# Kernel optimization log

Measured on AMD Instinct MI355X. Metric: run time of the kernel, lower is better.

The kernel has to match this reference:

```python
import jax, jax.numpy as jnp
import numpy as np

NUM_HEADS = 8
EPS = 1e-8

def setup_inputs() -> dict:
    key = jax.random.key(0)
    k1, k2, k3 = jax.random.split(key, 3)
    batch, L, dim = 2, 2048, 512
    B = jax.random.normal(k1, (batch, L, dim), dtype=jnp.float32)
    C = jax.random.normal(k2, (batch, L, dim), dtype=jnp.float32)
    S = jax.random.uniform(k3, (batch, L, dim), dtype=jnp.float32)
    return {"B": B, "C": C, "S": S}

def reference(B, C, S):
    batch, L, dim = B.shape
    H = NUM_HEADS
    d = dim // H
    # [b, H, L, d]
    Bh = B.reshape(batch, L, H, d).transpose(0, 2, 1, 3)
    Ch = C.reshape(batch, L, H, d).transpose(0, 2, 1, 3)
    Ah = S.reshape(batch, L, H, d).transpose(0, 2, 1, 3)
    # cum_A[0] = 1, cum_A[i] = prod_{k=1..i} A_k  (matches torch loop)
    cum_A = jnp.cumprod(Ah.at[:, :, 0, :].set(1.0), axis=2)
    ones = jnp.ones_like(cum_A[:, :, :1])
    # P[i] = cum_A[i-1] (P[0]=1): numerator of the product between j and i
    P = jnp.concatenate([ones, cum_A[:, :, :-1]], axis=2)
    # D[j] = cum_A[j-1] + eps for j>=1, D[0]=1 (j==0 branch has no eps)
    D = jnp.concatenate([ones, cum_A[:, :, :-1] + EPS], axis=2)
    # T_ij = sum_d C_i P_i B_j / D_j   for j < i
    T = jnp.einsum('bhid,bhjd->bhij', Ch * P, Bh / D)
    diag_vals = jnp.sum(Ch * Bh, axis=-1)  # T_ii = C_i . B_i
    idx = jnp.arange(L)
    strict_lower = idx[:, None] > idx[None, :]
    T = jnp.where(strict_lower, T, 0.0)
    T = T + diag_vals[:, :, :, None] * jnp.eye(L, dtype=T.dtype)
    # causal masking of strict upper triangle is already zero; use_softmax=False
    return T
```

## Files before the change

### kernel.cpp

```cpp
#include <hip/hip_runtime.h>
#include <hip/hip_bf16.h>

#define LL   2048
#define DIM  512
#define HD   64
#define BHN  16
#define NC   64
#define CH   32
#define EPSF 1e-8f

typedef __attribute__((ext_vector_type(8))) short bf16x8;
typedef __attribute__((ext_vector_type(4))) float f32x4;

__global__ __launch_bounds__(64) void chunkprod_kernel(const float* __restrict__ S,
                                                       float* __restrict__ U) {
    int c = blockIdx.x, bh = blockIdx.y;
    int b = bh >> 3, h = bh & 7;
    int d = threadIdx.x;
    int l0 = c * CH;
    size_t base = ((size_t)b * LL + l0) * DIM + h * HD + d;
    float p = 1.0f;
    for (int l = 0; l < CH; ++l) {
        float a = S[base + (size_t)l * DIM];
        if (l0 + l >= 1) p *= a;
    }
    U[((size_t)bh * NC + c) * HD + d] = p;
}

__global__ __launch_bounds__(64) void chunkscan_kernel(const float* __restrict__ U,
                                                       float* __restrict__ St) {
    int bh = blockIdx.x;
    int d = threadIdx.x;
    float p = 1.0f;
    for (int c = 0; c < NC; ++c) {
        size_t o = ((size_t)bh * NC + c) * HD + d;
        St[o] = p;
        p *= U[o];
    }
}

__global__ __launch_bounds__(64) void apply_kernel(const float* __restrict__ Bg,
                                                   const float* __restrict__ Cg,
                                                   const float* __restrict__ S,
                                                   const float* __restrict__ St,
                                                   __hip_bfloat16* __restrict__ X,
                                                   __hip_bfloat16* __restrict__ Y,
                                                   float* __restrict__ diag) {
    int c = blockIdx.x, bh = blockIdx.y;
    int b = bh >> 3, h = bh & 7;
    int d = threadIdx.x;
    int l0 = c * CH;
    size_t gbase = ((size_t)b * LL + l0) * DIM + h * HD + d;
    float p = St[((size_t)bh * NC + c) * HD + d];
    for (int l = 0; l < CH; ++l) {
        int gl = l0 + l;
        size_t gi = gbase + (size_t)l * DIM;
        float a = S[gi], bv = Bg[gi], cv = Cg[gi];
        float Dv = (gl == 0) ? 1.0f : (p + EPSF);
        size_t o = ((size_t)bh * LL + gl) * HD + d;
        X[o] = __float2bfloat16(cv * p);
        Y[o] = __float2bfloat16(bv / Dv);
        float tsum = cv * bv;
        #pragma unroll
        for (int off = 1; off < 64; off <<= 1) tsum += __shfl_xor(tsum, off);
        if (d == 0) diag[(size_t)bh * LL + gl] = tsum;
        if (gl >= 1) p *= a;
    }
}

__global__ __launch_bounds__(256) void gemm_kernel(const __hip_bfloat16* __restrict__ X,
                                                   const __hip_bfloat16* __restrict__ Y,
                                                   const float* __restrict__ diag,
                                                   float* __restrict__ out) {
    int tj = blockIdx.x, ti = blockIdx.y, bh = blockIdx.z;
    size_t obase = (size_t)bh * LL * LL;
    int i0 = ti * 128, j0 = tj * 128;
    int t = threadIdx.x;

    if (tj > ti) {
        float4 z = make_float4(0.f, 0.f, 0.f, 0.f);
        int col4 = t & 31, row0 = t >> 5;
        float* ob = out + obase + (size_t)i0 * LL + j0;
        #pragma unroll
        for (int r = 0; r < 16; ++r)
            *((float4*)(ob + (size_t)(row0 + 8 * r) * LL) + col4) = z;
        return;
    }

    __shared__ short Xs[128 * 64];
    __shared__ short Ys[128 * 64];

    {
        const float4* Xg4 = (const float4*)(X + ((size_t)bh * LL + i0) * HD);
        const float4* Yg4 = (const float4*)(Y + ((size_t)bh * LL + j0) * HD);
        int chunk = t & 7, r0 = t >> 3;
        int sc = (chunk ^ (r0 & 7)) * 8;
        #pragma unroll
        for (int p = 0; p < 4; ++p) {
            int row = r0 + 32 * p;
            float4 vx = Xg4[row * 8 + chunk];
            float4 vy = Yg4[row * 8 + chunk];
            *(float4*)&Xs[row * 64 + sc] = vx;
            *(float4*)&Ys[row * 64 + sc] = vy;
        }
    }
    __syncthreads();

    int lane = t & 63, wv = t >> 6;
    int wi = wv >> 1, wj = wv & 1;
    int l15 = lane & 15, q = lane >> 4;

    f32x4 acc[4][4] = {};
    #pragma unroll
    for (int kc = 0; kc < 2; ++kc) {
        bf16x8 af[4], bf[4];
        #pragma unroll
        for (int mt = 0; mt < 4; ++mt) {
            int row = 64 * wi + 16 * mt + l15;
            int sc = ((4 * kc + q) ^ (row & 7)) * 8;
            af[mt] = *(const bf16x8*)&Xs[row * 64 + sc];
        }
        #pragma unroll
        for (int nt = 0; nt < 4; ++nt) {
            int row = 64 * wj + 16 * nt + l15;
            int sc = ((4 * kc + q) ^ (row & 7)) * 8;
            bf[nt] = *(const bf16x8*)&Ys[row * 64 + sc];
        }
        #pragma unroll
        for (int mt = 0; mt < 4; ++mt)
            #pragma unroll
            for (int nt = 0; nt < 4; ++nt)
                acc[mt][nt] = __builtin_amdgcn_mfma_f32_16x16x32_bf16(
                    af[mt], bf[nt], acc[mt][nt], 0, 0, 0);
    }

    int i_base = i0 + 64 * wi, j_base = j0 + 64 * wj;
    if (tj < ti) {
        #pragma unroll
        for (int mt = 0; mt < 4; ++mt)
            #pragma unroll
            for (int reg = 0; reg < 4; ++reg) {
                int gi = i_base + 16 * mt + 4 * q + reg;
                float* ob = out + obase + (size_t)gi * LL + j_base;
                #pragma unroll
                for (int nt = 0; nt < 4; ++nt)
                    ob[16 * nt + l15] = acc[mt][nt][reg];
            }
    } else {
        #pragma unroll
        for (int mt = 0; mt < 4; ++mt)
            #pragma unroll
            for (int reg = 0; reg < 4; ++reg) {
                int gi = i_base + 16 * mt + 4 * q + reg;
                float dv = diag[(size_t)bh * LL + gi];
                float* ob = out + obase + (size_t)gi * LL + j_base;
                #pragma unroll
                for (int nt = 0; nt < 4; ++nt) {
                    int gj = j_base + 16 * nt + l15;
                    float v = acc[mt][nt][reg];
                    ob[16 * nt + l15] = (gj < gi) ? v : ((gj == gi) ? dv : 0.f);
                }
            }
    }
}

extern "C" void kernel_launch(void* const* d_in, const int* in_sizes, int n_in,
                              void* d_out, int out_size, void* d_ws, size_t ws_size,
                              hipStream_t stream) {
    const float* Bg = (const float*)d_in[0];
    const float* Cg = (const float*)d_in[1];
    const float* S  = (const float*)d_in[2];
    float* out = (float*)d_out;

    char* ws = (char*)d_ws;
    size_t xy_bytes = (size_t)BHN * LL * HD * sizeof(__hip_bfloat16);
    __hip_bfloat16* X = (__hip_bfloat16*)(ws);
    __hip_bfloat16* Y = (__hip_bfloat16*)(ws + xy_bytes);
    float* diag = (float*)(ws + 2 * xy_bytes);
    float* U    = (float*)(ws + 2 * xy_bytes + (size_t)BHN * LL * sizeof(float));
    float* St   = (float*)(ws + 2 * xy_bytes + (size_t)BHN * LL * sizeof(float)
                              + (size_t)BHN * NC * HD * sizeof(float));

    chunkprod_kernel<<<dim3(NC, BHN), 64, 0, stream>>>(S, U);
    chunkscan_kernel<<<BHN, 64, 0, stream>>>(U, St);
    apply_kernel<<<dim3(NC, BHN), 64, 0, stream>>>(Bg, Cg, S, St, X, Y, diag);
    gemm_kernel<<<dim3(16, 16, BHN), 256, 0, stream>>>(X, Y, diag, out);
}
```

Before: 329.1 us.

## Halve scan chunk size, parallelize chunk scan, split diag kernel, use nontemporal stores

Halves the chunk length and doubles the chunk count so the prefix and apply passes expose more blocks. The serial chunk scan becomes a two-level scan over 1024 threads using shared memory. The diagonal dot product moves out of apply_kernel into its own kernel, which adds a launch and a second read of B and C. Output stores in the GEMM, including the zero tiles, become nontemporal so the 256MB output write-out does not pollute the cache.

```diff
diff --git a/kernel.cpp b/kernel.cpp
--- a/kernel.cpp
+++ b/kernel.cpp
@@ -5,12 +5,20 @@
 #define DIM  512
 #define HD   64
 #define BHN  16
-#define NC   64
-#define CH   32
+#define NC   128
+#define CH   16
+#define GC   8
 #define EPSF 1e-8f
 
 typedef __attribute__((ext_vector_type(8))) short bf16x8;
 typedef __attribute__((ext_vector_type(4))) float f32x4;
+
+__device__ __forceinline__ void nt_store(float* p, float v) {
+    __builtin_nontemporal_store(v, p);
+}
+__device__ __forceinline__ void nt_store4(f32x4* p, f32x4 v) {
+    __builtin_nontemporal_store(v, p);
+}
 
 __global__ __launch_bounds__(64) void chunkprod_kernel(const float* __restrict__ S,
                                                        float* __restrict__ U) {
@@ -20,6 +28,7 @@
     int l0 = c * CH;
     size_t base = ((size_t)b * LL + l0) * DIM + h * HD + d;
     float p = 1.0f;
+    #pragma unroll
     for (int l = 0; l < CH; ++l) {
         float a = S[base + (size_t)l * DIM];
         if (l0 + l >= 1) p *= a;
@@ -27,16 +36,43 @@
     U[((size_t)bh * NC + c) * HD + d] = p;
 }
 
-__global__ __launch_bounds__(64) void chunkscan_kernel(const float* __restrict__ U,
-                                                       float* __restrict__ St) {
+__global__ __launch_bounds__(1024) void chunkscan_kernel(const float* __restrict__ U,
+                                                         float* __restrict__ St) {
     int bh = blockIdx.x;
-    int d = threadIdx.x;
-    float p = 1.0f;
-    for (int c = 0; c < NC; ++c) {
-        size_t o = ((size_t)bh * NC + c) * HD + d;
-        St[o] = p;
-        p *= U[o];
-    }
+    int t = threadIdx.x;
+    int g = t >> 6, d = t & 63;
+    int c0 = g * GC;
+    float u[GC];
+    float prod = 1.0f;
+    #pragma unroll
+    for (int k = 0; k < GC; ++k) {
+        u[k] = U[((size_t)bh * NC + c0 + k) * HD + d];
+        prod *= u[k];
+    }
+    __shared__ float Ls[16][64];
+    Ls[g][d] = prod;
+    __syncthreads();
+    float run = 1.0f;
+    for (int gg = 0; gg < g; ++gg) run *= Ls[gg][d];
+    #pragma unroll
+    for (int k = 0; k < GC; ++k) {
+        St[((size_t)bh * NC + c0 + k) * HD + d] = run;
+        run *= u[k];
+    }
+}
+
+__global__ __launch_bounds__(256) void diag_kernel(const float* __restrict__ Bg,
+                                                   const float* __restrict__ Cg,
+                                                   float* __restrict__ diag) {
+    int w = threadIdx.x >> 6, lane = threadIdx.x & 63;
+    int flat = blockIdx.x * 4 + w;
+    int bh = flat >> 11, l = flat & (LL - 1);
+    int b = bh >> 3, h = bh & 7;
+    size_t gi = ((size_t)b * LL + l) * DIM + h * HD + lane;
+    float tsum = Cg[gi] * Bg[gi];
+    #pragma unroll
+    for (int off = 1; off < 64; off <<= 1) tsum += __shfl_xor(tsum, off);
+    if (lane == 0) diag[(size_t)bh * LL + l] = tsum;
 }
 
 __global__ __launch_bounds__(64) void apply_kernel(const float* __restrict__ Bg,
@@ -44,14 +80,14 @@
                                                    const float* __restrict__ S,
                                                    const float* __restrict__ St,
                                                    __hip_bfloat16* __restrict__ X,
-                                                   __hip_bfloat16* __restrict__ Y,
-                                                   float* __restrict__ diag) {
+                                                   __hip_bfloat16* __restrict__ Y) {
     int c = blockIdx.x, bh = blockIdx.y;
     int b = bh >> 3, h = bh & 7;
     int d = threadIdx.x;
     int l0 = c * CH;
     size_t gbase = ((size_t)b * LL + l0) * DIM + h * HD + d;
     float p = St[((size_t)bh * NC + c) * HD + d];
+    #pragma unroll
     for (int l = 0; l < CH; ++l) {
         int gl = l0 + l;
         size_t gi = gbase + (size_t)l * DIM;
@@ -60,10 +96,6 @@
         size_t o = ((size_t)bh * LL + gl) * HD + d;
         X[o] = __float2bfloat16(cv * p);
         Y[o] = __float2bfloat16(bv / Dv);
-        float tsum = cv * bv;
-        #pragma unroll
-        for (int off = 1; off < 64; off <<= 1) tsum += __shfl_xor(tsum, off);
-        if (d == 0) diag[(size_t)bh * LL + gl] = tsum;
         if (gl >= 1) p *= a;
     }
 }
@@ -78,12 +110,12 @@
     int t = threadIdx.x;
 
     if (tj > ti) {
-        float4 z = make_float4(0.f, 0.f, 0.f, 0.f);
+        f32x4 z = {0.f, 0.f, 0.f, 0.f};
         int col4 = t & 31, row0 = t >> 5;
         float* ob = out + obase + (size_t)i0 * LL + j0;
         #pragma unroll
         for (int r = 0; r < 16; ++r)
-            *((float4*)(ob + (size_t)(row0 + 8 * r) * LL) + col4) = z;
+            nt_store4((f32x4*)(ob + (size_t)(row0 + 8 * r) * LL) + col4, z);
         return;
     }
 
@@ -91,17 +123,17 @@
     __shared__ short Ys[128 * 64];
 
     {
-        const float4* Xg4 = (const float4*)(X + ((size_t)bh * LL + i0) * HD);
-        const float4* Yg4 = (const float4*)(Y + ((size_t)bh * LL + j0) * HD);
+        const f32x4* Xg4 = (const f32x4*)(X + ((size_t)bh * LL + i0) * HD);
+        const f32x4* Yg4 = (const f32x4*)(Y + ((size_t)bh * LL + j0) * HD);
         int chunk = t & 7, r0 = t >> 3;
         int sc = (chunk ^ (r0 & 7)) * 8;
         #pragma unroll
         for (int p = 0; p < 4; ++p) {
             int row = r0 + 32 * p;
-            float4 vx = Xg4[row * 8 + chunk];
-            float4 vy = Yg4[row * 8 + chunk];
-            *(float4*)&Xs[row * 64 + sc] = vx;
-            *(float4*)&Ys[row * 64 + sc] = vy;
+            f32x4 vx = Xg4[row * 8 + chunk];
+            f32x4 vy = Yg4[row * 8 + chunk];
+            *(f32x4*)&Xs[row * 64 + sc] = vx;
+            *(f32x4*)&Ys[row * 64 + sc] = vy;
         }
     }
     __syncthreads();
@@ -144,7 +176,7 @@
                 float* ob = out + obase + (size_t)gi * LL + j_base;
                 #pragma unroll
                 for (int nt = 0; nt < 4; ++nt)
-                    ob[16 * nt + l15] = acc[mt][nt][reg];
+                    nt_store(ob + 16 * nt + l15, acc[mt][nt][reg]);
             }
     } else {
         #pragma unroll
@@ -158,7 +190,8 @@
                 for (int nt = 0; nt < 4; ++nt) {
                     int gj = j_base + 16 * nt + l15;
                     float v = acc[mt][nt][reg];
-                    ob[16 * nt + l15] = (gj < gi) ? v : ((gj == gi) ? dv : 0.f);
+                    nt_store(ob + 16 * nt + l15,
+                             (gj < gi) ? v : ((gj == gi) ? dv : 0.f));
                 }
             }
     }
@@ -182,7 +215,8 @@
                               + (size_t)BHN * NC * HD * sizeof(float));
 
     chunkprod_kernel<<<dim3(NC, BHN), 64, 0, stream>>>(S, U);
-    chunkscan_kernel<<<BHN, 64, 0, stream>>>(U, St);
-    apply_kernel<<<dim3(NC, BHN), 64, 0, stream>>>(Bg, Cg, S, St, X, Y, diag);
+    chunkscan_kernel<<<BHN, 1024, 0, stream>>>(U, St);
+    diag_kernel<<<(LL * BHN) / 4, 256, 0, stream>>>(Bg, Cg, diag);
+    apply_kernel<<<dim3(NC, BHN), 64, 0, stream>>>(Bg, Cg, S, St, X, Y);
     gemm_kernel<<<dim3(16, 16, BHN), 256, 0, stream>>>(X, Y, diag, out);
 }
```

After: 304.6 us. 7.4% less time.
